# Kernel optimization log

Hardware: AMD Instinct MI355X
Metric: run time of the kernel (lower is better)

The kernel has to match this reference:

```python
import jax, jax.numpy as jnp
import numpy as np

B, L, V, D_MODEL = 1, 2048, 32000, 768
N_LAYER, D_STATE, EXPAND, D_CONV = 2, 16, 2, 4
D_INNER = EXPAND * D_MODEL            # 1536
DT_RANK = -(-D_MODEL // D_STATE)      # ceil(768/16) = 48
EPS = 1e-5


def setup_inputs() -> dict:
    key = jax.random.key(0)
    ks = jax.random.split(key, 12)
    s = 0.02
    inp = {
        "input_ids": jax.random.randint(ks[0], (B, L), 0, V),
        "emb": jax.random.normal(ks[1], (V, D_MODEL), jnp.float32) * s,
        "norm_w": jnp.ones((N_LAYER, D_MODEL), jnp.float32),
        "in_proj_w": jax.random.normal(ks[2], (N_LAYER, D_MODEL, 2 * D_INNER), jnp.float32) * s,
        "conv_w": jax.random.normal(ks[3], (N_LAYER, D_INNER, 1, D_CONV), jnp.float32) * s,
        "conv_b": jnp.zeros((N_LAYER, D_INNER), jnp.float32),
        "x_proj_w": jax.random.normal(ks[4], (N_LAYER, D_INNER, DT_RANK + 2 * D_STATE), jnp.float32) * s,
        "dt_proj_w": jax.random.normal(ks[5], (N_LAYER, DT_RANK, D_INNER), jnp.float32) * s,
        "dt_proj_b": jax.random.normal(ks[6], (N_LAYER, D_INNER), jnp.float32) * s,
        "A_log": jnp.tile(jnp.log(jnp.arange(1, D_STATE + 1, dtype=jnp.float32)), (N_LAYER, D_INNER, 1)),
        "D": jnp.ones((N_LAYER, D_INNER), jnp.float32),
        "out_proj_w": jax.random.normal(ks[7], (N_LAYER, D_INNER, D_MODEL), jnp.float32) * s,
    }
    return inp


def _rmsnorm(x, w):
    return x * jax.lax.rsqrt(jnp.mean(x * x, axis=-1, keepdims=True) + EPS) * w


def _selective_scan(u, delta, A, Bm, Cm, D):
    # u, delta: (b,l,d); A: (d,n); Bm, Cm: (b,l,n); D: (d,)
    deltaA = jnp.exp(delta[..., None] * A)                     # (b,l,d,n)
    dBu = delta[..., None] * Bm[:, :, None, :] * u[..., None]  # (b,l,d,n)

    def comb(c1, c2):
        a1, b1 = c1
        a2, b2 = c2
        return a2 * a1, a2 * b1 + b2

    _, h = jax.lax.associative_scan(comb, (deltaA, dBu), axis=1)
    y = jnp.einsum('bldn,bln->bld', h, Cm)
    return y + u * D


def _mamba_block(x, in_proj_w, conv_w, conv_b, x_proj_w, dt_proj_w, dt_proj_b, A_log, D, out_proj_w):
    # x: (b,l,d_model)
    xz = x @ in_proj_w                                  # (b,l,2*d_inner)
    xr, res = jnp.split(xz, 2, axis=-1)
    # causal depthwise conv1d (left pad d_conv-1)
    xc = jax.lax.conv_general_dilated(
        jnp.swapaxes(xr, 1, 2), conv_w, (1,), [(D_CONV - 1, 0)],
        feature_group_count=D_INNER,
        dimension_numbers=('NCH', 'OIH', 'NCH'))
    xr = jax.nn.silu(jnp.swapaxes(xc + conv_b[:, None], 1, 2))  # (b,l,d_inner)

    A = -jnp.exp(A_log)                                 # (d_inner, n)
    x_dbl = xr @ x_proj_w                               # (b,l,dt_rank+2n)
    dt, Bm, Cm = jnp.split(x_dbl, [DT_RANK, DT_RANK + D_STATE], axis=-1)
    delta = jax.nn.softplus(dt @ dt_proj_w + dt_proj_b) # (b,l,d_inner)
    y = _selective_scan(xr, delta, A, Bm, Cm, D)
    return (y * jax.nn.silu(res)) @ out_proj_w


def reference(input_ids, emb, norm_w, in_proj_w, conv_w, conv_b, x_proj_w,
              dt_proj_w, dt_proj_b, A_log, D, out_proj_w):
    x = emb[input_ids]                                  # (b,l,d_model)
    for i in range(N_LAYER):
        x = x + _mamba_block(_rmsnorm(x, norm_w[i]), in_proj_w[i], conv_w[i],
                             conv_b[i], x_proj_w[i], dt_proj_w[i], dt_proj_b[i],
                             A_log[i], D[i], out_proj_w[i])
    return x
```

## Files before the change

### kernel.cpp

```cpp
#include <hip/hip_runtime.h>
#include <math.h>

#define L_SEQ 2048
#define DM    768
#define DI    1536
#define DTR   48
#define DST   16
#define XDW   80
#define NCH   64
#define LC    32
#define XPS   8
#define XPK   (DI / XPS)

typedef short bf16x8 __attribute__((ext_vector_type(8)));
typedef float f32x4  __attribute__((ext_vector_type(4)));

__device__ __forceinline__ float silu_f(float x) {
    return x / (1.0f + __expf(-x));
}

__device__ __forceinline__ short f2bf(float x) {
    union { float f; unsigned u; } v; v.f = x;
    unsigned r = v.u + 0x7fff + ((v.u >> 16) & 1);
    return (short)(r >> 16);
}

__global__ __launch_bounds__(256) void prep_kernel(
    const int*   __restrict__ ids,
    const float* __restrict__ emb,
    const float* __restrict__ in_proj_w,
    const float* __restrict__ out_proj_w,
    const float* __restrict__ x_proj_w,
    float* __restrict__ x,
    short* __restrict__ ipw_t, short* __restrict__ opw_t, short* __restrict__ xpw_t)
{
    __shared__ float tile[32 * 33];
    const int tid = threadIdx.x;
    int lx = tid & 31, ly = tid >> 5;

    for (int t = blockIdx.x; t < 7200; t += gridDim.x) {
        int layer = t >= 3600;
        int tt = t - layer * 3600;
        const float* src; short* dst; int K, N, txc;
        if (tt < 2304) {
            src = in_proj_w + (size_t)layer * DM * 2 * DI;
            dst = ipw_t + (size_t)layer * 2 * DI * DM;
            K = DM; N = 2 * DI; txc = 96;
        } else if (tt < 3456) {
            tt -= 2304;
            src = out_proj_w + (size_t)layer * DI * DM;
            dst = opw_t + (size_t)layer * DM * DI;
            K = DI; N = DM; txc = 24;
        } else {
            tt -= 3456;
            src = x_proj_w + (size_t)layer * DI * XDW;
            dst = xpw_t + (size_t)layer * XDW * DI;
            K = DI; N = XDW; txc = 3;
        }
        int n0 = (tt % txc) * 32, k0 = (tt / txc) * 32;
        __syncthreads();
        #pragma unroll
        for (int i = 0; i < 4; i++) {
            int nn = n0 + lx;
            tile[(ly + i * 8) * 33 + lx] =
                (nn < N) ? src[(size_t)(k0 + ly + i * 8) * N + nn] : 0.f;
        }
        __syncthreads();
        #pragma unroll
        for (int i = 0; i < 4; i++) {
            int nn = n0 + ly + i * 8;
            if (nn < N)
                dst[(size_t)nn * K + k0 + lx] = f2bf(tile[lx * 33 + ly + i * 8]);
        }
    }
    for (int idx = blockIdx.x * 256 + tid; idx < L_SEQ * (DM / 4); idx += gridDim.x * 256) {
        int row = idx / (DM / 4), col = idx % (DM / 4);
        ((float4*)x)[idx] = ((const float4*)emb)[(size_t)ids[row] * (DM / 4) + col];
    }
}

__global__ __launch_bounds__(256) void rmsnorm_kernel(
    const float* __restrict__ x, const float* __restrict__ w,
    short* __restrict__ out)
{
    int row = blockIdx.x;
    const float* xr = x + (size_t)row * DM;
    float s = 0.f;
    for (int i = threadIdx.x; i < DM; i += 256) { float v = xr[i]; s += v * v; }
    #pragma unroll
    for (int off = 32; off > 0; off >>= 1) s += __shfl_down(s, off, 64);
    __shared__ float ws[4];
    int wave = threadIdx.x >> 6, lane = threadIdx.x & 63;
    if (lane == 0) ws[wave] = s;
    __syncthreads();
    float tot = ws[0] + ws[1] + ws[2] + ws[3];
    float rs = rsqrtf(tot / (float)DM + 1e-5f);
    for (int i = threadIdx.x; i < DM; i += 256)
        out[(size_t)row * DM + i] = f2bf(xr[i] * rs * w[i]);
}

template <int MODE>
__global__ __launch_bounds__(256) void gemm_bf16_bt(
    const short* __restrict__ A, const short* __restrict__ Bt,
    float* __restrict__ C, int M, int N, int K)
{
    __shared__ short As[128 * 32];
    __shared__ short Bs[128 * 32];
    int tid = threadIdx.x, lane = tid & 63, w = tid >> 6;
    int wr = w >> 1, wc = w & 1;
    int brow = blockIdx.y * 128, bcol = blockIdx.x * 128;

    f32x4 acc[4][4] = {};

    for (int k0 = 0; k0 < K; k0 += 32) {
        #pragma unroll
        for (int i = 0; i < 2; i++) {
            int c = tid + i * 256;
            int r = c >> 2, q = c & 3;
            const short* ga = A  + (size_t)(brow + r) * K + k0 + q * 8;
            const short* gb = Bt + (size_t)(bcol + r) * K + k0 + q * 8;
            __builtin_amdgcn_global_load_lds(
                (const __attribute__((address_space(1))) void*)ga,
                (__attribute__((address_space(3))) void*)&As[r * 32 + q * 8],
                16, 0, 0);
            __builtin_amdgcn_global_load_lds(
                (const __attribute__((address_space(1))) void*)gb,
                (__attribute__((address_space(3))) void*)&Bs[r * 32 + q * 8],
                16, 0, 0);
        }
        __syncthreads();

        bf16x8 af[4], bfv[4];
        int kh = (lane >> 4) * 8;
        int ml = lane & 15;
        #pragma unroll
        for (int t = 0; t < 4; t++) {
            af[t]  = *(const bf16x8*)&As[(wr * 64 + t * 16 + ml) * 32 + kh];
            bfv[t] = *(const bf16x8*)&Bs[(wc * 64 + t * 16 + ml) * 32 + kh];
        }
        #pragma unroll
        for (int mt = 0; mt < 4; mt++)
            #pragma unroll
            for (int nt = 0; nt < 4; nt++)
                acc[mt][nt] = __builtin_amdgcn_mfma_f32_16x16x32_bf16(
                    af[mt], bfv[nt], acc[mt][nt], 0, 0, 0);
        __syncthreads();
    }

    int r0 = (lane >> 4) * 4, c0 = lane & 15;
    #pragma unroll
    for (int mt = 0; mt < 4; mt++)
        #pragma unroll
        for (int nt = 0; nt < 4; nt++)
            #pragma unroll
            for (int reg = 0; reg < 4; reg++) {
                int row = brow + wr * 64 + mt * 16 + r0 + reg;
                int col = bcol + wc * 64 + nt * 16 + c0;
                float v = acc[mt][nt][reg];
                if (MODE == 0) C[(size_t)row * N + col] = v;
                else           C[(size_t)row * N + col] += v;
            }
}

__global__ __launch_bounds__(256) void gemm_bf16_bt_n64(
    const short* __restrict__ A, const short* __restrict__ Bt,
    float* __restrict__ C, int M, int N, int K)
{
    __shared__ short As[128 * 32];
    __shared__ short Bs[64 * 32];
    int tid = threadIdx.x, lane = tid & 63, w = tid >> 6;
    int brow = blockIdx.y * 128, bcol = blockIdx.x * 64;

    f32x4 acc[2][4] = {};

    for (int k0 = 0; k0 < K; k0 += 32) {
        #pragma unroll
        for (int i = 0; i < 2; i++) {
            int c = tid + i * 256;
            int r = c >> 2, q = c & 3;
            const short* ga = A + (size_t)(brow + r) * K + k0 + q * 8;
            __builtin_amdgcn_global_load_lds(
                (const __attribute__((address_space(1))) void*)ga,
                (__attribute__((address_space(3))) void*)&As[r * 32 + q * 8],
                16, 0, 0);
        }
        {
            int r = tid >> 2, q = tid & 3;
            const short* gb = Bt + (size_t)(bcol + r) * K + k0 + q * 8;
            __builtin_amdgcn_global_load_lds(
                (const __attribute__((address_space(1))) void*)gb,
                (__attribute__((address_space(3))) void*)&Bs[r * 32 + q * 8],
                16, 0, 0);
        }
        __syncthreads();

        bf16x8 af[2], bfv[4];
        int kh = (lane >> 4) * 8;
        int ml = lane & 15;
        #pragma unroll
        for (int mt = 0; mt < 2; mt++)
            af[mt] = *(const bf16x8*)&As[(w * 32 + mt * 16 + ml) * 32 + kh];
        #pragma unroll
        for (int nt = 0; nt < 4; nt++)
            bfv[nt] = *(const bf16x8*)&Bs[(nt * 16 + ml) * 32 + kh];
        #pragma unroll
        for (int mt = 0; mt < 2; mt++)
            #pragma unroll
            for (int nt = 0; nt < 4; nt++)
                acc[mt][nt] = __builtin_amdgcn_mfma_f32_16x16x32_bf16(
                    af[mt], bfv[nt], acc[mt][nt], 0, 0, 0);
        __syncthreads();
    }

    int r0 = (lane >> 4) * 4, c0 = lane & 15;
    #pragma unroll
    for (int mt = 0; mt < 2; mt++)
        #pragma unroll
        for (int nt = 0; nt < 4; nt++)
            #pragma unroll
            for (int reg = 0; reg < 4; reg++) {
                int row = brow + w * 32 + mt * 16 + r0 + reg;
                int col = bcol + nt * 16 + c0;
                C[(size_t)row * N + col] += acc[mt][nt][reg];
            }
}

__global__ __launch_bounds__(256) void conv_silu_kernel(
    const float* __restrict__ xz, const float* __restrict__ w,
    const float* __restrict__ b, float* __restrict__ xr,
    short* __restrict__ xr_bf)
{
    int idx = blockIdx.x * 256 + threadIdx.x;
    if (idx >= L_SEQ * DI) return;
    int l = idx / DI, c = idx % DI;
    float4 wc = ((const float4*)w)[c];
    const float* col = xz + c;
    float acc = b[c];
    if (l >= 3) {
        acc += wc.x * col[(size_t)(l - 3) * (2 * DI)]
             + wc.y * col[(size_t)(l - 2) * (2 * DI)]
             + wc.z * col[(size_t)(l - 1) * (2 * DI)]
             + wc.w * col[(size_t)l * (2 * DI)];
    } else {
        const float wv[4] = {wc.x, wc.y, wc.z, wc.w};
        for (int k = 0; k < 4; k++) {
            int ls = l - 3 + k;
            if (ls >= 0) acc += wv[k] * col[(size_t)ls * (2 * DI)];
        }
    }
    float v = silu_f(acc);
    xr[idx] = v;
    xr_bf[idx] = f2bf(v);
}

__global__ __launch_bounds__(256) void xproj_splitk(
    const short* __restrict__ xr_bf,
    const short* __restrict__ xpw_t,
    float* __restrict__ part)
{
    int w = threadIdx.x >> 6, lane = threadIdx.x & 63;
    int r0 = blockIdx.x * 64 + w * 16;
    int k0 = blockIdx.y * XPK;
    int ml = lane & 15, kh = (lane >> 4) * 8;

    f32x4 acc[5] = {};
    for (int ks = 0; ks < XPK; ks += 32) {
        bf16x8 a = *(const bf16x8*)&xr_bf[(size_t)(r0 + ml) * DI + k0 + ks + kh];
        #pragma unroll
        for (int t = 0; t < 5; t++) {
            bf16x8 b = *(const bf16x8*)&xpw_t[(size_t)(t * 16 + ml) * DI + k0 + ks + kh];
            acc[t] = __builtin_amdgcn_mfma_f32_16x16x32_bf16(a, b, acc[t], 0, 0, 0);
        }
    }
    float* po = part + (size_t)blockIdx.y * L_SEQ * XDW;
    int r_base = r0 + (lane >> 4) * 4;
    #pragma unroll
    for (int t = 0; t < 5; t++)
        #pragma unroll
        for (int reg = 0; reg < 4; reg++)
            po[(size_t)(r_base + reg) * XDW + t * 16 + ml] = acc[t][reg];
}

__global__ __launch_bounds__(256) void dtproj_fused(
    const float* __restrict__ xpart, const float* __restrict__ dpw,
    const float* __restrict__ dpb, float* __restrict__ delta,
    float* __restrict__ xdbl_bc)
{
    __shared__ __align__(16) float As_f[16 * 68];
    __shared__ __align__(16) float Bs_f[16 * 68];
    int tid = threadIdx.x;
    int ty = tid >> 4, tx = tid & 15;
    int t = blockIdx.x;
    int bcol = (t % 24) * 64;
    int brow = (t / 24) * 64;

    float acc[4][4] = {};
    for (int k0 = 0; k0 < 48; k0 += 16) {
        __syncthreads();
        #pragma unroll
        for (int i = 0; i < 4; i++) {
            int idx = tid + i * 256;
            int m = idx >> 4, k = idx & 15;
            float s = 0.f;
            #pragma unroll
            for (int p = 0; p < XPS; p++)
                s += xpart[((size_t)p * L_SEQ + brow + m) * XDW + k0 + k];
            As_f[k * 68 + m] = s;
        }
        #pragma unroll
        for (int i = 0; i < 4; i++) {
            int idx = tid + i * 256;
            int k = idx >> 6, n = idx & 63;
            Bs_f[k * 68 + n] = dpw[(size_t)(k0 + k) * DI + bcol + n];
        }
        __syncthreads();
        #pragma unroll
        for (int k = 0; k < 16; k++) {
            float4 av = *(const float4*)&As_f[k * 68 + ty * 4];
            float4 bv = *(const float4*)&Bs_f[k * 68 + tx * 4];
            float a4[4] = {av.x, av.y, av.z, av.w};
            float b4[4] = {bv.x, bv.y, bv.z, bv.w};
            #pragma unroll
            for (int i = 0; i < 4; i++)
                #pragma unroll
                for (int jj = 0; jj < 4; jj++)
                    acc[i][jj] += a4[i] * b4[jj];
        }
    }
    #pragma unroll
    for (int i = 0; i < 4; i++) {
        int row = brow + ty * 4 + i;
        #pragma unroll
        for (int jj = 0; jj < 4; jj++) {
            int col = bcol + tx * 4 + jj;
            float v = acc[i][jj] + dpb[col];
            delta[(size_t)row * DI + col] = (v > 20.f) ? v : log1pf(__expf(v));
        }
    }
    if (t % 24 == 0) {
        for (int e = tid; e < 64 * 32; e += 256) {
            int r = e >> 5, cc = e & 31;
            float s = 0.f;
            #pragma unroll
            for (int p = 0; p < XPS; p++)
                s += xpart[((size_t)p * L_SEQ + brow + r) * XDW + DTR + cc];
            xdbl_bc[(size_t)(brow + r) * 32 + cc] = s;
        }
    }
}

__global__ __launch_bounds__(256) void scan_passA(
    const float* __restrict__ delta, const float* __restrict__ xr,
    const float* __restrict__ xdbl_bc, const float* __restrict__ al,
    float* __restrict__ aprod, float* __restrict__ hfin)
{
    int d = blockIdx.x * 256 + threadIdx.x;
    int c = blockIdx.y;

    float Aloc[DST], h[DST], P[DST];
    #pragma unroll
    for (int n4 = 0; n4 < DST; n4 += 4) {
        float4 alv = *(const float4*)&al[(size_t)d * DST + n4];
        Aloc[n4 + 0] = -__expf(alv.x); Aloc[n4 + 1] = -__expf(alv.y);
        Aloc[n4 + 2] = -__expf(alv.z); Aloc[n4 + 3] = -__expf(alv.w);
    }
    #pragma unroll
    for (int n = 0; n < DST; n++) { h[n] = 0.f; P[n] = 1.f; }

    int l0 = c * LC;
    for (int l = l0; l < l0 + LC; l++) {
        float dl = delta[(size_t)l * DI + d];
        float ul = xr[(size_t)l * DI + d];
        float du = dl * ul;
        float Bv[DST];
        const float4* B4 = (const float4*)(xdbl_bc + (size_t)l * 32);
        *(float4*)&Bv[0] = B4[0]; *(float4*)&Bv[4]  = B4[1];
        *(float4*)&Bv[8] = B4[2]; *(float4*)&Bv[12] = B4[3];
        #pragma unroll
        for (int n = 0; n < DST; n++) {
            float da = __expf(dl * Aloc[n]);
            h[n] = h[n] * da + du * Bv[n];
            P[n] *= da;
        }
    }
    size_t base = ((size_t)c * DI + d) * DST;
    #pragma unroll
    for (int n = 0; n < DST; n += 4) {
        *(float4*)&aprod[base + n] = *(float4*)&P[n];
        *(float4*)&hfin[base + n]  = *(float4*)&h[n];
    }
}

__global__ __launch_bounds__(256) void scan_passB(
    const float* __restrict__ aprod, const float* __restrict__ hfin,
    float* __restrict__ hin)
{
    int idx = blockIdx.x * 256 + threadIdx.x;
    if (idx >= DI * DST) return;
    float cur = 0.f;
    for (int c = 0; c < NCH; c++) {
        size_t o = (size_t)c * DI * DST + idx;
        hin[o] = cur;
        cur = hfin[o] + aprod[o] * cur;
    }
}

__global__ __launch_bounds__(256) void scan_passC(
    const float* __restrict__ delta, const float* __restrict__ xr,
    const float* __restrict__ xdbl_bc, const float* __restrict__ al,
    const float* __restrict__ dpp, const float* __restrict__ hin,
    const float* __restrict__ xz, short* __restrict__ y2)
{
    int d = blockIdx.x * 256 + threadIdx.x;
    int c = blockIdx.y;

    float Aloc[DST], h[DST];
    #pragma unroll
    for (int n4 = 0; n4 < DST; n4 += 4) {
        float4 alv = *(const float4*)&al[(size_t)d * DST + n4];
        Aloc[n4 + 0] = -__expf(alv.x); Aloc[n4 + 1] = -__expf(alv.y);
        Aloc[n4 + 2] = -__expf(alv.z); Aloc[n4 + 3] = -__expf(alv.w);
    }
    size_t base = ((size_t)c * DI + d) * DST;
    #pragma unroll
    for (int n = 0; n < DST; n += 4)
        *(float4*)&h[n] = *(const float4*)&hin[base + n];
    float Dd = dpp[d];

    int l0 = c * LC;
    for (int l = l0; l < l0 + LC; l++) {
        float dl = delta[(size_t)l * DI + d];
        float ul = xr[(size_t)l * DI + d];
        float du = dl * ul;
        float Bv[DST], Cv[DST];
        const float4* B4 = (const float4*)(xdbl_bc + (size_t)l * 32);
        const float4* C4 = (const float4*)(xdbl_bc + (size_t)l * 32 + 16);
        *(float4*)&Bv[0] = B4[0]; *(float4*)&Bv[4]  = B4[1];
        *(float4*)&Bv[8] = B4[2]; *(float4*)&Bv[12] = B4[3];
        *(float4*)&Cv[0] = C4[0]; *(float4*)&Cv[4]  = C4[1];
        *(float4*)&Cv[8] = C4[2]; *(float4*)&Cv[12] = C4[3];
        float y = 0.f;
        #pragma unroll
        for (int n = 0; n < DST; n++) {
            float da = __expf(dl * Aloc[n]);
            h[n] = h[n] * da + du * Bv[n];
            y += h[n] * Cv[n];
        }
        y += ul * Dd;
        float r = xz[(size_t)l * (2 * DI) + DI + d];
        y2[(size_t)l * DI + d] = f2bf(y * silu_f(r));
    }
}

extern "C" void kernel_launch(void* const* d_in, const int* in_sizes, int n_in,
                              void* d_out, int out_size, void* d_ws, size_t ws_size,
                              hipStream_t stream)
{
    const int*   ids       = (const int*)d_in[0];
    const float* emb       = (const float*)d_in[1];
    const float* norm_w    = (const float*)d_in[2];
    const float* in_proj_w = (const float*)d_in[3];
    const float* conv_w    = (const float*)d_in[4];
    const float* conv_b    = (const float*)d_in[5];
    const float* x_proj_w  = (const float*)d_in[6];
    const float* dt_proj_w = (const float*)d_in[7];
    const float* dt_proj_b = (const float*)d_in[8];
    const float* A_log     = (const float*)d_in[9];
    const float* Dp        = (const float*)d_in[10];
    const float* out_proj_w= (const float*)d_in[11];

    float* x = (float*)d_out;

    char* wsb = (char*)d_ws;
    auto alloc_f = [&](size_t n) { float* p = (float*)wsb; wsb += n * 4; return p; };
    auto alloc_s = [&](size_t n) { short* p = (short*)wsb; wsb += ((n * 2 + 15) & ~15ull); return p; };

    float* xz      = alloc_f((size_t)L_SEQ * 2 * DI);
    float* xr      = alloc_f((size_t)L_SEQ * DI);
    float* delta   = alloc_f((size_t)L_SEQ * DI);
    float* xpart   = alloc_f((size_t)XPS * L_SEQ * XDW);
    float* xdbl_bc = alloc_f((size_t)L_SEQ * 32);
    float* aprod   = alloc_f((size_t)NCH * DI * DST);
    float* hfin    = alloc_f((size_t)NCH * DI * DST);
    float* hin     = alloc_f((size_t)NCH * DI * DST);
    short* xn_bf   = alloc_s((size_t)L_SEQ * DM);
    short* y2_bf   = alloc_s((size_t)L_SEQ * DI);
    short* xr_bf   = alloc_s((size_t)L_SEQ * DI);
    short* ipw_t   = alloc_s((size_t)2 * 2 * DI * DM);
    short* opw_t   = alloc_s((size_t)2 * DM * DI);
    short* xpw_t   = alloc_s((size_t)2 * XDW * DI);

    prep_kernel<<<1024, 256, 0, stream>>>(
        ids, emb, in_proj_w, out_proj_w, x_proj_w, x, ipw_t, opw_t, xpw_t);

    for (int layer = 0; layer < 2; layer++) {
        const float* nw   = norm_w    + (size_t)layer * DM;
        const float* cw   = conv_w    + (size_t)layer * DI * 4;
        const float* cb   = conv_b    + (size_t)layer * DI;
        const float* dpw  = dt_proj_w + (size_t)layer * DTR * DI;
        const float* dpb  = dt_proj_b + (size_t)layer * DI;
        const float* al   = A_log     + (size_t)layer * DI * DST;
        const float* dpp  = Dp        + (size_t)layer * DI;
        const short* ipwt = ipw_t + (size_t)layer * 2 * DI * DM;
        const short* opwt = opw_t + (size_t)layer * DM * DI;
        const short* xpwt = xpw_t + (size_t)layer * XDW * DI;

        rmsnorm_kernel<<<L_SEQ, 256, 0, stream>>>(x, nw, xn_bf);

        gemm_bf16_bt<0><<<dim3(2 * DI / 128, L_SEQ / 128), 256, 0, stream>>>(
            xn_bf, ipwt, xz, L_SEQ, 2 * DI, DM);

        conv_silu_kernel<<<(L_SEQ * DI) / 256, 256, 0, stream>>>(xz, cw, cb, xr, xr_bf);

        xproj_splitk<<<dim3(L_SEQ / 64, XPS), 256, 0, stream>>>(xr_bf, xpwt, xpart);

        dtproj_fused<<<768, 256, 0, stream>>>(xpart, dpw, dpb, delta, xdbl_bc);

        scan_passA<<<dim3(DI / 256, NCH), 256, 0, stream>>>(
            delta, xr, xdbl_bc, al, aprod, hfin);
        scan_passB<<<(DI * DST) / 256, 256, 0, stream>>>(aprod, hfin, hin);
        scan_passC<<<dim3(DI / 256, NCH), 256, 0, stream>>>(
            delta, xr, xdbl_bc, al, dpp, hin, xz, y2_bf);

        gemm_bf16_bt_n64<<<dim3(DM / 64, L_SEQ / 128), 256, 0, stream>>>(
            y2_bf, opwt, x, L_SEQ, DM, DI);
    }
}
```

Measured before the change: 482.1 us.

## Fuse conv+silu into x_proj, fold first rmsnorm into prep, drop fp32 xr

The depthwise conv and SiLU are now computed inside the x_proj split-K kernel. Each block stages a 64-row bf16 tile in LDS and also writes xr_bf, which removes one launch and the fp32 xr buffer. The scan passes read bf16 xr instead of fp32, halving that traffic but lowering the precision of u. The first layer's RMSNorm moves into the prep kernel, which now uses one block per token row and drops one more launch. The convxproj grid is small (32x8 blocks), and each block computes the conv with strided global reads, so parallelism may suffer.

After: 513.6 us. 6.5% more time.

```diff
diff --git a/kernel.cpp b/kernel.cpp
--- a/kernel.cpp
+++ b/kernel.cpp
@@ -11,6 +11,7 @@
 #define LC    32
 #define XPS   8
 #define XPK   (DI / XPS)
+#define XPAD  200
 
 typedef short bf16x8 __attribute__((ext_vector_type(8)));
 typedef float f32x4  __attribute__((ext_vector_type(4)));
@@ -25,19 +26,56 @@
     return (short)(r >> 16);
 }
 
+__device__ __forceinline__ float bf2f(short s) {
+    union { float f; unsigned u; } v;
+    v.u = ((unsigned)(unsigned short)s) << 16;
+    return v.f;
+}
+
 __global__ __launch_bounds__(256) void prep_kernel(
     const int*   __restrict__ ids,
     const float* __restrict__ emb,
+    const float* __restrict__ norm_w,
     const float* __restrict__ in_proj_w,
     const float* __restrict__ out_proj_w,
     const float* __restrict__ x_proj_w,
     float* __restrict__ x,
+    short* __restrict__ xn_bf,
     short* __restrict__ ipw_t, short* __restrict__ opw_t, short* __restrict__ xpw_t)
 {
     __shared__ float tile[32 * 33];
+    __shared__ float wred[4];
     const int tid = threadIdx.x;
+
+    {
+        int row = blockIdx.x;
+        int tok = ids[row];
+        float4 v4 = make_float4(0.f, 0.f, 0.f, 0.f);
+        if (tid < DM / 4) {
+            v4 = ((const float4*)emb)[(size_t)tok * (DM / 4) + tid];
+            ((float4*)x)[(size_t)row * (DM / 4) + tid] = v4;
+        }
+        float s = v4.x * v4.x + v4.y * v4.y + v4.z * v4.z + v4.w * v4.w;
+        #pragma unroll
+        for (int off = 32; off > 0; off >>= 1) s += __shfl_down(s, off, 64);
+        int wave = tid >> 6, lane = tid & 63;
+        if (lane == 0) wred[wave] = s;
+        __syncthreads();
+        float tot = wred[0] + wred[1] + wred[2] + wred[3];
+        float rs = rsqrtf(tot / (float)DM + 1e-5f);
+        if (tid < DM / 4) {
+            int i = tid * 4;
+            short4 o;
+            o.x = f2bf(v4.x * rs * norm_w[i + 0]);
+            o.y = f2bf(v4.y * rs * norm_w[i + 1]);
+            o.z = f2bf(v4.z * rs * norm_w[i + 2]);
+            o.w = f2bf(v4.w * rs * norm_w[i + 3]);
+            ((short4*)xn_bf)[(size_t)row * (DM / 4) + tid] = o;
+        }
+        __syncthreads();
+    }
+
     int lx = tid & 31, ly = tid >> 5;
-
     for (int t = blockIdx.x; t < 7200; t += gridDim.x) {
         int layer = t >= 3600;
         int tt = t - layer * 3600;
@@ -73,10 +111,6 @@
                 dst[(size_t)nn * K + k0 + lx] = f2bf(tile[lx * 33 + ly + i * 8]);
         }
     }
-    for (int idx = blockIdx.x * 256 + tid; idx < L_SEQ * (DM / 4); idx += gridDim.x * 256) {
-        int row = idx / (DM / 4), col = idx % (DM / 4);
-        ((float4*)x)[idx] = ((const float4*)emb)[(size_t)ids[row] * (DM / 4) + col];
-    }
 }
 
 __global__ __launch_bounds__(256) void rmsnorm_kernel(
@@ -99,7 +133,6 @@
         out[(size_t)row * DM + i] = f2bf(xr[i] * rs * w[i]);
 }
 
-template <int MODE>
 __global__ __launch_bounds__(256) void gemm_bf16_bt(
     const short* __restrict__ A, const short* __restrict__ Bt,
     float* __restrict__ C, int M, int N, int K)
@@ -156,9 +189,7 @@
             for (int reg = 0; reg < 4; reg++) {
                 int row = brow + wr * 64 + mt * 16 + r0 + reg;
                 int col = bcol + wc * 64 + nt * 16 + c0;
-                float v = acc[mt][nt][reg];
-                if (MODE == 0) C[(size_t)row * N + col] = v;
-                else           C[(size_t)row * N + col] += v;
+                C[(size_t)row * N + col] = acc[mt][nt][reg];
             }
 }
 
@@ -225,60 +256,61 @@
             }
 }
 
-__global__ __launch_bounds__(256) void conv_silu_kernel(
-    const float* __restrict__ xz, const float* __restrict__ w,
-    const float* __restrict__ b, float* __restrict__ xr,
-    short* __restrict__ xr_bf)
-{
-    int idx = blockIdx.x * 256 + threadIdx.x;
-    if (idx >= L_SEQ * DI) return;
-    int l = idx / DI, c = idx % DI;
-    float4 wc = ((const float4*)w)[c];
-    const float* col = xz + c;
-    float acc = b[c];
-    if (l >= 3) {
-        acc += wc.x * col[(size_t)(l - 3) * (2 * DI)]
-             + wc.y * col[(size_t)(l - 2) * (2 * DI)]
-             + wc.z * col[(size_t)(l - 1) * (2 * DI)]
-             + wc.w * col[(size_t)l * (2 * DI)];
-    } else {
-        const float wv[4] = {wc.x, wc.y, wc.z, wc.w};
-        for (int k = 0; k < 4; k++) {
-            int ls = l - 3 + k;
-            if (ls >= 0) acc += wv[k] * col[(size_t)ls * (2 * DI)];
-        }
-    }
-    float v = silu_f(acc);
-    xr[idx] = v;
-    xr_bf[idx] = f2bf(v);
-}
-
-__global__ __launch_bounds__(256) void xproj_splitk(
-    const short* __restrict__ xr_bf,
-    const short* __restrict__ xpw_t,
-    float* __restrict__ part)
-{
-    int w = threadIdx.x >> 6, lane = threadIdx.x & 63;
-    int r0 = blockIdx.x * 64 + w * 16;
-    int k0 = blockIdx.y * XPK;
+__global__ __launch_bounds__(256) void convxproj_kernel(
+    const float* __restrict__ xz, const float* __restrict__ cw,
+    const float* __restrict__ cb, const short* __restrict__ xpw_t,
+    short* __restrict__ xr_bf, float* __restrict__ part)
+{
+    __shared__ __align__(16) short lds[64 * XPAD];
+    const int tid = threadIdx.x;
+    int rg = blockIdx.x;
+    int sp = blockIdx.y;
+    int l0 = rg * 64;
+    int k0 = sp * XPK;
+
+    for (int e = tid; e < 64 * XPK; e += 256) {
+        int ll = e / XPK, cc = e % XPK;
+        int l = l0 + ll, c = k0 + cc;
+        float4 wc4 = ((const float4*)cw)[c];
+        const float* col = xz + c;
+        float acc = cb[c];
+        if (l >= 3) {
+            acc += wc4.x * col[(size_t)(l - 3) * (2 * DI)]
+                 + wc4.y * col[(size_t)(l - 2) * (2 * DI)]
+                 + wc4.z * col[(size_t)(l - 1) * (2 * DI)]
+                 + wc4.w * col[(size_t)l * (2 * DI)];
+        } else {
+            const float wv[4] = {wc4.x, wc4.y, wc4.z, wc4.w};
+            for (int k = 0; k < 4; k++) {
+                int ls = l - 3 + k;
+                if (ls >= 0) acc += wv[k] * col[(size_t)ls * (2 * DI)];
+            }
+        }
+        short b = f2bf(silu_f(acc));
+        lds[ll * XPAD + cc] = b;
+        xr_bf[(size_t)l * DI + c] = b;
+    }
+    __syncthreads();
+
+    int w = tid >> 6, lane = tid & 63;
     int ml = lane & 15, kh = (lane >> 4) * 8;
-
-    f32x4 acc[5] = {};
+    int rl = w * 16 + ml;
+    f32x4 acc5[5] = {};
     for (int ks = 0; ks < XPK; ks += 32) {
-        bf16x8 a = *(const bf16x8*)&xr_bf[(size_t)(r0 + ml) * DI + k0 + ks + kh];
-        #pragma unroll
-        for (int t = 0; t < 5; t++) {
-            bf16x8 b = *(const bf16x8*)&xpw_t[(size_t)(t * 16 + ml) * DI + k0 + ks + kh];
-            acc[t] = __builtin_amdgcn_mfma_f32_16x16x32_bf16(a, b, acc[t], 0, 0, 0);
-        }
-    }
-    float* po = part + (size_t)blockIdx.y * L_SEQ * XDW;
-    int r_base = r0 + (lane >> 4) * 4;
-    #pragma unroll
-    for (int t = 0; t < 5; t++)
+        bf16x8 a = *(const bf16x8*)&lds[rl * XPAD + ks + kh];
+        #pragma unroll
+        for (int t5 = 0; t5 < 5; t5++) {
+            bf16x8 b = *(const bf16x8*)&xpw_t[(size_t)(t5 * 16 + ml) * DI + k0 + ks + kh];
+            acc5[t5] = __builtin_amdgcn_mfma_f32_16x16x32_bf16(a, b, acc5[t5], 0, 0, 0);
+        }
+    }
+    float* po = part + (size_t)sp * L_SEQ * XDW;
+    int rb = l0 + w * 16 + (lane >> 4) * 4;
+    #pragma unroll
+    for (int t5 = 0; t5 < 5; t5++)
         #pragma unroll
         for (int reg = 0; reg < 4; reg++)
-            po[(size_t)(r_base + reg) * XDW + t * 16 + ml] = acc[t][reg];
+            po[(size_t)(rb + reg) * XDW + t5 * 16 + ml] = acc5[t5][reg];
 }
 
 __global__ __launch_bounds__(256) void dtproj_fused(
@@ -350,7 +382,7 @@
 }
 
 __global__ __launch_bounds__(256) void scan_passA(
-    const float* __restrict__ delta, const float* __restrict__ xr,
+    const float* __restrict__ delta, const short* __restrict__ xr_bf,
     const float* __restrict__ xdbl_bc, const float* __restrict__ al,
     float* __restrict__ aprod, float* __restrict__ hfin)
 {
@@ -370,7 +402,7 @@
     int l0 = c * LC;
     for (int l = l0; l < l0 + LC; l++) {
         float dl = delta[(size_t)l * DI + d];
-        float ul = xr[(size_t)l * DI + d];
+        float ul = bf2f(xr_bf[(size_t)l * DI + d]);
         float du = dl * ul;
         float Bv[DST];
         const float4* B4 = (const float4*)(xdbl_bc + (size_t)l * 32);
@@ -406,7 +438,7 @@
 }
 
 __global__ __launch_bounds__(256) void scan_passC(
-    const float* __restrict__ delta, const float* __restrict__ xr,
+    const float* __restrict__ delta, const short* __restrict__ xr_bf,
     const float* __restrict__ xdbl_bc, const float* __restrict__ al,
     const float* __restrict__ dpp, const float* __restrict__ hin,
     const float* __restrict__ xz, short* __restrict__ y2)
@@ -430,7 +462,7 @@
     int l0 = c * LC;
     for (int l = l0; l < l0 + LC; l++) {
         float dl = delta[(size_t)l * DI + d];
-        float ul = xr[(size_t)l * DI + d];
+        float ul = bf2f(xr_bf[(size_t)l * DI + d]);
         float du = dl * ul;
         float Bv[DST], Cv[DST];
         const float4* B4 = (const float4*)(xdbl_bc + (size_t)l * 32);
@@ -476,7 +508,6 @@
     auto alloc_s = [&](size_t n) { short* p = (short*)wsb; wsb += ((n * 2 + 15) & ~15ull); return p; };
 
     float* xz      = alloc_f((size_t)L_SEQ * 2 * DI);
-    float* xr      = alloc_f((size_t)L_SEQ * DI);
     float* delta   = alloc_f((size_t)L_SEQ * DI);
     float* xpart   = alloc_f((size_t)XPS * L_SEQ * XDW);
     float* xdbl_bc = alloc_f((size_t)L_SEQ * 32);
@@ -490,8 +521,9 @@
     short* opw_t   = alloc_s((size_t)2 * DM * DI);
     short* xpw_t   = alloc_s((size_t)2 * XDW * DI);
 
-    prep_kernel<<<1024, 256, 0, stream>>>(
-        ids, emb, in_proj_w, out_proj_w, x_proj_w, x, ipw_t, opw_t, xpw_t);
+    prep_kernel<<<L_SEQ, 256, 0, stream>>>(
+        ids, emb, norm_w, in_proj_w, out_proj_w, x_proj_w,
+        x, xn_bf, ipw_t, opw_t, xpw_t);
 
     for (int layer = 0; layer < 2; layer++) {
         const float* nw   = norm_w    + (size_t)layer * DM;
@@ -505,22 +537,22 @@
         const short* opwt = opw_t + (size_t)layer * DM * DI;
         const short* xpwt = xpw_t + (size_t)layer * XDW * DI;
 
-        rmsnorm_kernel<<<L_SEQ, 256, 0, stream>>>(x, nw, xn_bf);
-
-        gemm_bf16_bt<0><<<dim3(2 * DI / 128, L_SEQ / 128), 256, 0, stream>>>(
+        if (layer == 1)
+            rmsnorm_kernel<<<L_SEQ, 256, 0, stream>>>(x, nw, xn_bf);
+
+        gemm_bf16_bt<<<dim3(2 * DI / 128, L_SEQ / 128), 256, 0, stream>>>(
             xn_bf, ipwt, xz, L_SEQ, 2 * DI, DM);
 
-        conv_silu_kernel<<<(L_SEQ * DI) / 256, 256, 0, stream>>>(xz, cw, cb, xr, xr_bf);
-
-        xproj_splitk<<<dim3(L_SEQ / 64, XPS), 256, 0, stream>>>(xr_bf, xpwt, xpart);
+        convxproj_kernel<<<dim3(32, XPS), 256, 0, stream>>>(
+            xz, cw, cb, xpwt, xr_bf, xpart);
 
         dtproj_fused<<<768, 256, 0, stream>>>(xpart, dpw, dpb, delta, xdbl_bc);
 
         scan_passA<<<dim3(DI / 256, NCH), 256, 0, stream>>>(
-            delta, xr, xdbl_bc, al, aprod, hfin);
+            delta, xr_bf, xdbl_bc, al, aprod, hfin);
         scan_passB<<<(DI * DST) / 256, 256, 0, stream>>>(aprod, hfin, hin);
         scan_passC<<<dim3(DI / 256, NCH), 256, 0, stream>>>(
-            delta, xr, xdbl_bc, al, dpp, hin, xz, y2_bf);
+            delta, xr_bf, xdbl_bc, al, dpp, hin, xz, y2_bf);
 
         gemm_bf16_bt_n64<<<dim3(DM / 64, L_SEQ / 128), 256, 0, stream>>>(
             y2_bf, opwt, x, L_SEQ, DM, DI);
```
